# Kernel optimization log

Hardware: AMD Instinct MI355X
Metric: run time of the kernel (lower is better)

The kernel has to match this reference:

```python
import jax, jax.numpy as jnp
import numpy as np
from jax.scipy.linalg import lu_factor, lu_solve

DT = 0.1          # dt
EPS = 0.01        # epsilon
STEPS = 40        # max sweep iterations
TOL = 1e-4        # convergence tolerance


def setup_inputs() -> dict:
    key = jax.random.key(0)
    ks = jax.random.split(key, 9)
    B, D_IN, U, D_OUT = 2048, 1024, 1024, 1000
    def lin(kw, kb, out_f, in_f):
        bound = 1.0 / np.sqrt(in_f)
        W = jax.random.uniform(kw, (out_f, in_f), jnp.float32, -bound, bound)
        b = jax.random.uniform(kb, (out_f,), jnp.float32, -bound, bound)
        return W, b
    x = jax.random.normal(ks[0], (B, D_IN), jnp.float32)
    W_in, b_in = lin(ks[1], ks[2], U, D_IN)
    W1, b1 = lin(ks[3], ks[4], U, U)
    W2, b2 = lin(ks[5], ks[6], U, U)
    W_out, b_out = lin(ks[7], ks[8], D_OUT, U)
    return {"x": x, "W_in": W_in, "b_in": b_in, "W1": W1, "b1": b1,
            "W2": W2, "b2": b2, "W_out": W_out, "b_out": b_out}


def _make_A(W):
    # A = [[I, dt*W], [-dt*W^T, (1+dt/eps)*I]], shape [2u, 2u]
    u = W.shape[0]
    I = jnp.eye(u, dtype=W.dtype)
    return jnp.block([[I, DT * W], [-DT * W.T, (1.0 + DT / EPS) * I]])


def _run_sweep(z_in, rhs1, rhs2, A1, A2):
    # Gauss-Seidel-like sweeping: z1 = A1^{-1}(rhs1+z_in); z2 = A2^{-1}(rhs2+z1)
    # A is identical across the batch, so factor once and solve for all rhs.
    lu1 = lu_factor(A1)
    lu2 = lu_factor(A2)
    r1 = rhs1 + z_in  # constant across sweeps
    def cond(c):
        _, _, err, step = c
        return (step < STEPS) & (err > TOL)
    def body(c):
        z1, z2, _, step = c
        y1 = lu_solve(lu1, r1.T).T
        e1 = jnp.mean(jnp.linalg.norm(z1 - y1, axis=1))
        y2 = lu_solve(lu2, (rhs2 + y1).T).T
        e2 = jnp.mean(jnp.linalg.norm(z2 - y2, axis=1))
        return y1, y2, 0.5 * (e1 + e2), step + 1
    z1, z2, _, _ = jax.lax.while_loop(
        cond, body, (z_in, z_in, jnp.float32(10.0), jnp.int32(0)))
    return z1, z2


@jax.custom_vjp
def _hook(z, A):
    # Forward identity; backward replaces grad g with A^{-T} g (per-row),
    # mirroring the torch register_hook(torch.solve(grad, J^T)).
    return z

def _hook_fwd(z, A):
    return z, A

def _hook_bwd(A, g):
    gz = jnp.linalg.solve(A.T, g.T).T
    return gz, jnp.zeros_like(A)

_hook.defvjp(_hook_fwd, _hook_bwd)


def _implicit(z_in_blk, z_l, W, b, A):
    u = W.shape[0]
    u_in, v_in = z_in_blk[:, :u], z_in_blk[:, u:]
    u_out = u_in + DT * b - DT * (z_l[:, u:] @ W.T)
    v_out = v_in + DT * (z_l[:, :u] @ W) - (DT / EPS) * (z_l[:, u:] - jnp.tanh(u_in))
    z = jnp.concatenate([u_out, v_out], axis=1)
    return _hook(z, jax.lax.stop_gradient(A))


def reference(x, W_in, b_in, W1, b1, W2, b2, W_out, b_out):
    sg = jax.lax.stop_gradient
    u = W1.shape[0]
    B = x.shape[0]
    h = x @ W_in.T + b_in                       # [B, u]
    z_in = jnp.concatenate([h, jnp.tanh(h)], axis=1)  # [B, 2u]
    A1 = _make_A(W1)
    A2 = _make_A(W2)
    # relax rhs = [dt*b, dt/eps * tanh(u_in)] (built from z_in for both blocks)
    tz = (DT / EPS) * jnp.tanh(z_in[:, :u])
    rhs1 = jnp.concatenate([jnp.broadcast_to(DT * b1, (B, u)), tz], axis=1)
    rhs2 = jnp.concatenate([jnp.broadcast_to(DT * b2, (B, u)), tz], axis=1)
    # sweep loop runs under no_grad in the original -> stop_gradient everywhere
    z1, z2 = _run_sweep(sg(z_in), sg(rhs1), sg(rhs2), sg(A1), sg(A2))
    z = _implicit(z_in, z1, W1, b1, A1)
    z = _implicit(z, z2, W2, b2, A2)
    logits = z[:, :u] @ W_out.T + b_out
    return jax.nn.softmax(logits, axis=1)
```

## Files before the change

### kernel.cpp

```cpp
#include <hip/hip_runtime.h>


typedef short bf16x8 __attribute__((ext_vector_type(8)));
typedef float f32x4 __attribute__((ext_vector_type(4)));

#define M1 1048576

__device__ __forceinline__ unsigned short f2b(float f) {
  union { float f; unsigned int u; } v; v.f = f;
  unsigned int u = v.u;
  return (unsigned short)((u + 0x7FFFu + ((u >> 16) & 1u)) >> 16);
}

__device__ __forceinline__ void gload16(const void* g, void* l) {
  __builtin_amdgcn_global_load_lds(
      (const __attribute__((address_space(1))) unsigned int*)g,
      (__attribute__((address_space(3))) unsigned int*)l, 16, 0, 0);
}

template <int MODE, int NKT>
__device__ __forceinline__ void gemm64(
    const unsigned short* __restrict__ A, int lda,
    const unsigned short* __restrict__ B, int ldb,
    int bx, int by,
    const float* bias0, const float* bias1, const float* src0,
    float* dstf0, float* dstf1,
    unsigned short* dstbf, int ldc, unsigned short* dstbf2,
    short (*As)[4096], short (*Bs)[4096]) {
  const int tid = threadIdx.x;
  const int lane = tid & 63;
  const int wid = tid >> 6;
  const int wr = wid >> 1;
  const int wc = wid & 1;
  const int m0 = bx * 64;
  const int n0 = by * 64;
  const int l15 = lane & 15;
  const int kb = lane >> 4;

  const int sr = tid >> 3;
  const int sg = ((tid & 7) - sr) & 7;
  const unsigned short* Asrc = A + (size_t)(m0 + sr) * lda + sg * 8;
  const unsigned short* Bsrc = B + (size_t)(n0 + sr) * ldb + sg * 8;
  const size_t a32 = (size_t)32 * lda;
  const size_t b32 = (size_t)32 * ldb;
  const int o0 = tid * 8;
  const int o1 = 2048 + tid * 8;

  f32x4 acc[2][2];
#pragma unroll
  for (int f = 0; f < 2; ++f)
#pragma unroll
    for (int g = 0; g < 2; ++g) acc[f][g] = (f32x4){0.f, 0.f, 0.f, 0.f};

#define STG(kt, buf)                                  \
  do {                                                \
    gload16(Asrc + (kt) * 64, &As[(buf)][o0]);        \
    gload16(Asrc + a32 + (kt) * 64, &As[(buf)][o1]);  \
    gload16(Bsrc + (kt) * 64, &Bs[(buf)][o0]);        \
    gload16(Bsrc + b32 + (kt) * 64, &Bs[(buf)][o1]);  \
  } while (0)

#define CMP(kt)                                                                \
  do {                                                                         \
    const int cb = (kt) & 3;                                                   \
    bf16x8 av[2][2], bv[2][2];                                                 \
    _Pragma("unroll") for (int f = 0; f < 2; ++f) {                            \
      const int ra = wr * 32 + f * 16 + l15;                                   \
      _Pragma("unroll") for (int ks = 0; ks < 2; ++ks) {                       \
        const int qa = (ks * 4 + kb + l15) & 7;                                \
        av[f][ks] = *reinterpret_cast<const bf16x8*>(&As[cb][ra * 64 + qa * 8]); \
      }                                                                        \
    }                                                                          \
    _Pragma("unroll") for (int g = 0; g < 2; ++g) {                            \
      const int rb = wc * 32 + g * 16 + l15;                                   \
      _Pragma("unroll") for (int ks = 0; ks < 2; ++ks) {                       \
        const int qb2 = (ks * 4 + kb + l15) & 7;                               \
        bv[g][ks] = *reinterpret_cast<const bf16x8*>(&Bs[cb][rb * 64 + qb2 * 8]); \
      }                                                                        \
    }                                                                          \
    _Pragma("unroll") for (int ks = 0; ks < 2; ++ks)                           \
        _Pragma("unroll") for (int f = 0; f < 2; ++f)                          \
            _Pragma("unroll") for (int g = 0; g < 2; ++g)                      \
                acc[f][g] = __builtin_amdgcn_mfma_f32_16x16x32_bf16(           \
                    av[f][ks], bv[g][ks], acc[f][g], 0, 0, 0);                 \
  } while (0)

  STG(0, 0);
  STG(1, 1);

#pragma unroll
  for (int s = 0; s < NKT / 2; ++s) {
    const int k0 = 2 * s;
    asm volatile("s_waitcnt vmcnt(0)" ::: "memory");
    __builtin_amdgcn_sched_barrier(0);
    __builtin_amdgcn_s_barrier();
    __builtin_amdgcn_sched_barrier(0);
    if (k0 + 2 < NKT) STG(k0 + 2, (k0 + 2) & 3);
    if (k0 + 3 < NKT) STG(k0 + 3, (k0 + 3) & 3);
    __builtin_amdgcn_s_setprio(1);
    CMP(k0);
    CMP(k0 + 1);
    __builtin_amdgcn_s_setprio(0);
  }
#undef STG
#undef CMP

#pragma unroll
  for (int f = 0; f < 2; ++f) {
#pragma unroll
    for (int g = 0; g < 2; ++g) {
#pragma unroll
      for (int j = 0; j < 4; ++j) {
        int m = m0 + wr * 32 + f * 16 + kb * 4 + j;
        int n = n0 + wc * 32 + g * 16 + l15;
        size_t fidx = (size_t)m * 1024 + n;
        size_t cidx = (size_t)m * ldc + n;
        float v = acc[f][g][j];
        if (MODE == 0) {
          dstbf[cidx] = f2b(v);
        } else if (MODE == 1) {
          float h = v + bias0[n];
          float thv = tanhf(h);
          float r = h + 0.1f * bias1[n];
          dstf0[fidx] = r;
          dstf1[fidx] = thv;
          dstbf[cidx] = f2b(r);
        } else if (MODE == 2) {
          dstbf[cidx] = f2b(11.0f * src0[fidx] + 0.1f * v);
        } else if (MODE == 4) {
          float r = src0[fidx] + 0.1f * bias0[n] - 0.1f * v;
          dstf0[fidx] = r;
          dstbf[cidx] = f2b(0.1f * r);
        } else if (MODE == 5) {
          dstbf[cidx] = f2b(10.0f * src0[fidx] + v);
        } else if (MODE == 7) {
          dstbf[cidx] = f2b(src0[fidx] - 0.1f * v);
        } else if (MODE == 8) {
          dstf0[fidx] = v + bias0[n];
        } else {
          float q = (m == n ? (1.0f / 11.0f) : 0.0f) - (0.01f / 121.0f) * v;
          unsigned short qq = f2b(q);
          dstbf[cidx] = qq;
          if (dstbf2) dstbf2[(size_t)m * 2048 + n] = qq;
        }
      }
    }
  }
}

__device__ __forceinline__ void map512(int b, int& bx, int& by) {
  bx = ((b & 7) << 2) | ((b >> 3) & 3);
  by = b >> 5;
}
__device__ __forceinline__ void map256(int r, int& bx, int& by) {
  bx = ((r & 7) << 1) | ((r >> 3) & 1);
  by = (r >> 4) & 15;
}
__device__ __forceinline__ void map512k2(int b, int& bx, int& by) {
  const int x = b & 7;
  const int j = b >> 3;
  bx = ((x & 3) << 3) | (j & 7);
  by = ((x >> 2) << 3) | (j >> 3);
}

__global__ __launch_bounds__(256) void k_D2(
    const unsigned short* __restrict__ xb, const unsigned short* __restrict__ winb,
    const unsigned short* __restrict__ wtb,
    const float* __restrict__ b_in, const float* __restrict__ b1,
    float* __restrict__ r1u, float* __restrict__ th,
    unsigned short* __restrict__ zb0, unsigned short* __restrict__ qb,
    unsigned short* __restrict__ bcat) {
  __shared__ short As[4][4096];
  __shared__ short Bs[4][4096];
  const int b = blockIdx.x;
  int bx, by;
  if (b < 512) {
    map512(b, bx, by);
    gemm64<1, 16>(xb, 1024, winb, 1024, bx, by, b_in, b1, nullptr,
                  r1u, th, zb0, 1024, nullptr, As, Bs);
  } else {
    int r = b - 512;
    const int z = r >> 8;
    map256(r & 255, bx, by);
    const unsigned short* wt = wtb + (size_t)z * M1;
    gemm64<9, 16>(wt, 1024, wt, 1024, bx, by, nullptr, nullptr, nullptr,
                  nullptr, nullptr, qb + (size_t)z * M1, 1024,
                  z == 0 ? bcat : nullptr, As, Bs);
  }
}

__global__ __launch_bounds__(256) void k_D3(
    const unsigned short* __restrict__ wb, const unsigned short* __restrict__ qb,
    const unsigned short* __restrict__ zb0, const unsigned short* __restrict__ wtb,
    const float* __restrict__ th,
    unsigned short* __restrict__ a1b, unsigned short* __restrict__ a2b,
    unsigned short* __restrict__ zcat) {
  __shared__ short As[4][4096];
  __shared__ short Bs[4][4096];
  const int b = blockIdx.x;
  int bx, by;
  if (b < 512) {
    const int z = b >> 8;
    map256(b & 255, bx, by);
    gemm64<0, 16>(wb + (size_t)z * M1, 1024, qb + (size_t)z * M1, 1024, bx, by,
                  nullptr, nullptr, nullptr, nullptr, nullptr,
                  z == 0 ? a1b : a2b, 1024, nullptr, As, Bs);
  } else {
    map512(b - 512, bx, by);
    gemm64<2, 16>(zb0, 1024, wtb, 1024, bx, by, nullptr, nullptr, th,
                  nullptr, nullptr, zcat, 2048, nullptr, As, Bs);
  }
}

__global__ __launch_bounds__(256) void k_D4(
    const unsigned short* __restrict__ zcat, const unsigned short* __restrict__ a1b,
    const float* __restrict__ b2, const float* __restrict__ r1u,
    float* __restrict__ r2u, unsigned short* __restrict__ zcat_hi) {
  __shared__ short As[4][4096];
  __shared__ short Bs[4][4096];
  int bx, by;
  map512(blockIdx.x, bx, by);
  gemm64<4, 16>(zcat, 2048, a1b, 1024, bx, by, b2, nullptr, r1u,
                r2u, nullptr, zcat_hi, 2048, nullptr, As, Bs);
}

__global__ __launch_bounds__(256) void k_D5(
    const unsigned short* __restrict__ zcat, const unsigned short* __restrict__ bcat,
    const float* __restrict__ th, unsigned short* __restrict__ zb2) {
  __shared__ short As[4][4096];
  __shared__ short Bs[4][4096];
  int bx, by;
  map512k2(blockIdx.x, bx, by);
  gemm64<5, 32>(zcat, 2048, bcat, 2048, bx, by, nullptr, nullptr, th,
                nullptr, nullptr, zb2, 1024, nullptr, As, Bs);
}

__global__ __launch_bounds__(256) void k_D6(
    const unsigned short* __restrict__ zb2, const unsigned short* __restrict__ a2b,
    const float* __restrict__ r2u, unsigned short* __restrict__ zb3) {
  __shared__ short As[4][4096];
  __shared__ short Bs[4][4096];
  int bx, by;
  map512(blockIdx.x, bx, by);
  gemm64<7, 16>(zb2, 1024, a2b, 1024, bx, by, nullptr, nullptr, r2u,
                nullptr, nullptr, zb3, 1024, nullptr, As, Bs);
}

__global__ __launch_bounds__(256) void k_D7(
    const unsigned short* __restrict__ zb3, const unsigned short* __restrict__ woutb,
    const float* __restrict__ boutp, float* __restrict__ lgts) {
  __shared__ short As[4][4096];
  __shared__ short Bs[4][4096];
  int bx, by;
  map512(blockIdx.x, bx, by);
  gemm64<8, 16>(zb3, 1024, woutb, 1024, bx, by, boutp, nullptr, nullptr,
                lgts, nullptr, nullptr, 1024, nullptr, As, Bs);
}

__global__ __launch_bounds__(256) void k_prep(
    const float* __restrict__ x, const float* __restrict__ Win,
    const float* __restrict__ W1, const float* __restrict__ W2,
    const float* __restrict__ Wout, const float* __restrict__ bout,
    unsigned short* __restrict__ xb, unsigned short* __restrict__ winb,
    unsigned short* __restrict__ wb, unsigned short* __restrict__ wtb,
    unsigned short* __restrict__ woutb, float* __restrict__ boutp,
    unsigned short* __restrict__ bcat) {
  __shared__ float tile[32][33];
  const int b = blockIdx.x;
  const int tid = threadIdx.x;
  if (b < 2048) {
    const int isW2 = (b >> 10) & 1;
    const float* W = isW2 ? W2 : W1;
    unsigned short* Wb = wb + ((size_t)isW2 << 20);
    unsigned short* WTb = wtb + ((size_t)isW2 << 20);
    const int rem = b & 1023;
    const int tbx = rem & 31, tby = rem >> 5;
    const int tx = tid & 31, ty = tid >> 5;
#pragma unroll
    for (int i = ty; i < 32; i += 8) {
      float v = W[(size_t)(tby * 32 + i) * 1024 + tbx * 32 + tx];
      tile[i][tx] = v;
      Wb[(size_t)(tby * 32 + i) * 1024 + tbx * 32 + tx] = f2b(v);
    }
    __syncthreads();
#pragma unroll
    for (int i = ty; i < 32; i += 8) {
      unsigned short t2 = f2b(tile[tx][i]);
      int rr = tbx * 32 + i, cc = tby * 32 + tx;
      WTb[(size_t)rr * 1024 + cc] = t2;
      if (isW2) bcat[(size_t)rr * 2048 + 1024 + cc] = t2;
    }
  } else if (b < 4096) {
    int i = (b - 2048) * 256 + tid;
    float4 v = ((const float4*)x)[i];
    ((ushort4*)xb)[i] = (ushort4){f2b(v.x), f2b(v.y), f2b(v.z), f2b(v.w)};
  } else if (b < 5120) {
    int i = (b - 4096) * 256 + tid;
    float4 v = ((const float4*)Win)[i];
    ((ushort4*)winb)[i] = (ushort4){f2b(v.x), f2b(v.y), f2b(v.z), f2b(v.w)};
  } else if (b < 6144) {
    int i = (b - 5120) * 256 + tid;
    ushort4 o = (ushort4){0, 0, 0, 0};
    if ((i >> 8) < 1000) {
      float4 v = ((const float4*)Wout)[i];
      o = (ushort4){f2b(v.x), f2b(v.y), f2b(v.z), f2b(v.w)};
    }
    ((ushort4*)woutb)[i] = o;
  } else {
    for (int j = tid; j < 1024; j += 256) boutp[j] = (j < 1000) ? bout[j] : 0.0f;
  }
}

__global__ __launch_bounds__(256) void k_softmax(const float* __restrict__ lg,
                                                 float* __restrict__ out) {
  const int r = blockIdx.x;
  const float4* p4 = (const float4*)(lg + (size_t)r * 1024);
  float* q = out + (size_t)r * 1000;
  const int tid = threadIdx.x;
  const int lane = tid & 63;
  const int w = tid >> 6;
  __shared__ float redm[4];
  __shared__ float reds[4];
  float m = -3.0e38f;
  for (int i = tid; i < 250; i += 256) {
    float4 v = p4[i];
    m = fmaxf(fmaxf(fmaxf(m, v.x), fmaxf(v.y, v.z)), v.w);
  }
#pragma unroll
  for (int o = 32; o > 0; o >>= 1) m = fmaxf(m, __shfl_xor(m, o));
  if (lane == 0) redm[w] = m;
  __syncthreads();
  m = fmaxf(fmaxf(redm[0], redm[1]), fmaxf(redm[2], redm[3]));
  float s = 0.0f;
  for (int i = tid; i < 250; i += 256) {
    float4 v = p4[i];
    float e0 = __expf(v.x - m), e1 = __expf(v.y - m);
    float e2 = __expf(v.z - m), e3 = __expf(v.w - m);
    float4 e = {e0, e1, e2, e3};
    *reinterpret_cast<float4*>(q + i * 4) = e;
    s += e0 + e1 + e2 + e3;
  }
#pragma unroll
  for (int o = 32; o > 0; o >>= 1) s += __shfl_xor(s, o);
  if (lane == 0) reds[w] = s;
  __syncthreads();
  float inv = 1.0f / (reds[0] + reds[1] + reds[2] + reds[3]);
  for (int i = tid; i < 250; i += 256) {
    float4 e = *reinterpret_cast<const float4*>(q + i * 4);
    e.x *= inv; e.y *= inv; e.z *= inv; e.w *= inv;
    *reinterpret_cast<float4*>(q + i * 4) = e;
  }
}

extern "C" void kernel_launch(void* const* d_in, const int* in_sizes, int n_in,
                              void* d_out, int out_size, void* d_ws, size_t ws_size,
                              hipStream_t stream) {
  const float* x = (const float*)d_in[0];
  const float* W_in = (const float*)d_in[1];
  const float* b_in = (const float*)d_in[2];
  const float* W1 = (const float*)d_in[3];
  const float* b1 = (const float*)d_in[4];
  const float* W2 = (const float*)d_in[5];
  const float* b2 = (const float*)d_in[6];
  const float* W_out = (const float*)d_in[7];
  const float* b_out = (const float*)d_in[8];
  float* out = (float*)d_out;

  const size_t Bm = 2048, U = 1024;
  char* ws = (char*)d_ws;
  size_t off = 0;
  auto alloc = [&](size_t bytes) -> void* {
    void* p = ws + off;
    off += (bytes + 255) & ~(size_t)255;
    return p;
  };
  unsigned short* xb = (unsigned short*)alloc(Bm * U * 2);
  unsigned short* winb = (unsigned short*)alloc((size_t)M1 * 2);
  unsigned short* wb = (unsigned short*)alloc(2 * (size_t)M1 * 2);
  unsigned short* wtb = (unsigned short*)alloc(2 * (size_t)M1 * 2);
  unsigned short* qb = (unsigned short*)alloc(2 * (size_t)M1 * 2);
  unsigned short* a1b = (unsigned short*)alloc((size_t)M1 * 2);
  unsigned short* a2b = (unsigned short*)alloc((size_t)M1 * 2);
  unsigned short* bcat = (unsigned short*)alloc(2 * (size_t)M1 * 2);
  unsigned short* woutb = (unsigned short*)alloc((size_t)M1 * 2);
  float* boutp = (float*)alloc(U * 4);
  unsigned short* zb0 = (unsigned short*)alloc(Bm * U * 2);
  unsigned short* zcat = (unsigned short*)alloc(Bm * 2 * U * 2);
  unsigned short* zb2 = (unsigned short*)alloc(Bm * U * 2);
  unsigned short* zb3 = (unsigned short*)alloc(Bm * U * 2);
  float* r1u = (float*)alloc(Bm * U * 4);
  float* th = (float*)alloc(Bm * U * 4);
  float* r2u = (float*)alloc(Bm * U * 4);
  float* lgts = (float*)alloc(Bm * U * 4);

  k_prep<<<6145, 256, 0, stream>>>(x, W_in, W1, W2, W_out, b_out,
                                   xb, winb, wb, wtb, woutb, boutp, bcat);
  k_D2<<<1024, 256, 0, stream>>>(xb, winb, wtb, b_in, b1, r1u, th, zb0, qb, bcat);
  k_D3<<<1024, 256, 0, stream>>>(wb, qb, zb0, wtb, th, a1b, a2b, zcat);
  k_D4<<<512, 256, 0, stream>>>(zcat, a1b, b2, r1u, r2u, zcat + 1024);
  k_D5<<<512, 256, 0, stream>>>(zcat, bcat, th, zb2);
  k_D6<<<512, 256, 0, stream>>>(zb2, a2b, r2u, zb3);
  k_D7<<<512, 256, 0, stream>>>(zb3, woutb, boutp, lgts);
  k_softmax<<<2048, 256, 0, stream>>>(lgts, out);
}
```

Before: 105.7 us.

## Split K across wave pairs in 64x64 GEMM tile with LDS reduction

Warps were previously laid out 2x2 over the output tile, each covering 32x32 and all of K. Now each wave pair splits the 64-wide K slice in half, with each wave covering a 64x32 output region over its half of K. The partial sums are then reduced through LDS before a single wave pair runs the epilogue. This cuts the number of LDS fragment reads for each MFMA, since each A fragment is reused across two B fragments and each B across four A fragments. The cost is more accumulator registers, an extra LDS round trip with two barriers, and an epilogue run by only half the waves.

```diff
diff --git a/kernel.cpp b/kernel.cpp
--- a/kernel.cpp
+++ b/kernel.cpp
@@ -30,7 +30,7 @@
   const int tid = threadIdx.x;
   const int lane = tid & 63;
   const int wid = tid >> 6;
-  const int wr = wid >> 1;
+  const int ksw = wid >> 1;
   const int wc = wid & 1;
   const int m0 = bx * 64;
   const int n0 = by * 64;
@@ -46,9 +46,9 @@
   const int o0 = tid * 8;
   const int o1 = 2048 + tid * 8;
 
-  f32x4 acc[2][2];
-#pragma unroll
-  for (int f = 0; f < 2; ++f)
+  f32x4 acc[4][2];
+#pragma unroll
+  for (int f = 0; f < 4; ++f)
 #pragma unroll
     for (int g = 0; g < 2; ++g) acc[f][g] = (f32x4){0.f, 0.f, 0.f, 0.f};
 
@@ -63,26 +63,21 @@
 #define CMP(kt)                                                                \
   do {                                                                         \
     const int cb = (kt) & 3;                                                   \
-    bf16x8 av[2][2], bv[2][2];                                                 \
-    _Pragma("unroll") for (int f = 0; f < 2; ++f) {                            \
-      const int ra = wr * 32 + f * 16 + l15;                                   \
-      _Pragma("unroll") for (int ks = 0; ks < 2; ++ks) {                       \
-        const int qa = (ks * 4 + kb + l15) & 7;                                \
-        av[f][ks] = *reinterpret_cast<const bf16x8*>(&As[cb][ra * 64 + qa * 8]); \
-      }                                                                        \
+    bf16x8 av[4], bv[2];                                                       \
+    _Pragma("unroll") for (int f = 0; f < 4; ++f) {                            \
+      const int ra = f * 16 + l15;                                             \
+      const int qa = (ksw * 4 + kb + l15) & 7;                                 \
+      av[f] = *reinterpret_cast<const bf16x8*>(&As[cb][ra * 64 + qa * 8]);     \
     }                                                                          \
     _Pragma("unroll") for (int g = 0; g < 2; ++g) {                            \
       const int rb = wc * 32 + g * 16 + l15;                                   \
-      _Pragma("unroll") for (int ks = 0; ks < 2; ++ks) {                       \
-        const int qb2 = (ks * 4 + kb + l15) & 7;                               \
-        bv[g][ks] = *reinterpret_cast<const bf16x8*>(&Bs[cb][rb * 64 + qb2 * 8]); \
-      }                                                                        \
+      const int qb2 = (ksw * 4 + kb + l15) & 7;                                \
+      bv[g] = *reinterpret_cast<const bf16x8*>(&Bs[cb][rb * 64 + qb2 * 8]);    \
     }                                                                          \
-    _Pragma("unroll") for (int ks = 0; ks < 2; ++ks)                           \
-        _Pragma("unroll") for (int f = 0; f < 2; ++f)                          \
-            _Pragma("unroll") for (int g = 0; g < 2; ++g)                      \
-                acc[f][g] = __builtin_amdgcn_mfma_f32_16x16x32_bf16(           \
-                    av[f][ks], bv[g][ks], acc[f][g], 0, 0, 0);                 \
+    _Pragma("unroll") for (int f = 0; f < 4; ++f)                              \
+        _Pragma("unroll") for (int g = 0; g < 2; ++g)                          \
+            acc[f][g] = __builtin_amdgcn_mfma_f32_16x16x32_bf16(               \
+                av[f], bv[g], acc[f][g], 0, 0, 0);                             \
   } while (0)
 
   STG(0, 0);
@@ -105,43 +100,61 @@
 #undef STG
 #undef CMP
 
-#pragma unroll
-  for (int f = 0; f < 2; ++f) {
-#pragma unroll
-    for (int g = 0; g < 2; ++g) {
-#pragma unroll
-      for (int j = 0; j < 4; ++j) {
-        int m = m0 + wr * 32 + f * 16 + kb * 4 + j;
-        int n = n0 + wc * 32 + g * 16 + l15;
-        size_t fidx = (size_t)m * 1024 + n;
-        size_t cidx = (size_t)m * ldc + n;
-        float v = acc[f][g][j];
-        if (MODE == 0) {
-          dstbf[cidx] = f2b(v);
-        } else if (MODE == 1) {
-          float h = v + bias0[n];
-          float thv = tanhf(h);
-          float r = h + 0.1f * bias1[n];
-          dstf0[fidx] = r;
-          dstf1[fidx] = thv;
-          dstbf[cidx] = f2b(r);
-        } else if (MODE == 2) {
-          dstbf[cidx] = f2b(11.0f * src0[fidx] + 0.1f * v);
-        } else if (MODE == 4) {
-          float r = src0[fidx] + 0.1f * bias0[n] - 0.1f * v;
-          dstf0[fidx] = r;
-          dstbf[cidx] = f2b(0.1f * r);
-        } else if (MODE == 5) {
-          dstbf[cidx] = f2b(10.0f * src0[fidx] + v);
-        } else if (MODE == 7) {
-          dstbf[cidx] = f2b(src0[fidx] - 0.1f * v);
-        } else if (MODE == 8) {
-          dstf0[fidx] = v + bias0[n];
-        } else {
-          float q = (m == n ? (1.0f / 11.0f) : 0.0f) - (0.01f / 121.0f) * v;
-          unsigned short qq = f2b(q);
-          dstbf[cidx] = qq;
-          if (dstbf2) dstbf2[(size_t)m * 2048 + n] = qq;
+  f32x4* fbuf = reinterpret_cast<f32x4*>(&As[0][0]);
+  __syncthreads();
+  if (ksw == 1) {
+#pragma unroll
+    for (int f = 0; f < 4; ++f)
+#pragma unroll
+      for (int g = 0; g < 2; ++g)
+        fbuf[wc * 512 + (f * 2 + g) * 64 + lane] = acc[f][g];
+  }
+  __syncthreads();
+  if (ksw == 0) {
+#pragma unroll
+    for (int f = 0; f < 4; ++f)
+#pragma unroll
+      for (int g = 0; g < 2; ++g)
+        acc[f][g] += fbuf[wc * 512 + (f * 2 + g) * 64 + lane];
+
+#pragma unroll
+    for (int f = 0; f < 4; ++f) {
+#pragma unroll
+      for (int g = 0; g < 2; ++g) {
+#pragma unroll
+        for (int j = 0; j < 4; ++j) {
+          int m = m0 + f * 16 + kb * 4 + j;
+          int n = n0 + wc * 32 + g * 16 + l15;
+          size_t fidx = (size_t)m * 1024 + n;
+          size_t cidx = (size_t)m * ldc + n;
+          float v = acc[f][g][j];
+          if (MODE == 0) {
+            dstbf[cidx] = f2b(v);
+          } else if (MODE == 1) {
+            float h = v + bias0[n];
+            float thv = tanhf(h);
+            float r = h + 0.1f * bias1[n];
+            dstf0[fidx] = r;
+            dstf1[fidx] = thv;
+            dstbf[cidx] = f2b(r);
+          } else if (MODE == 2) {
+            dstbf[cidx] = f2b(11.0f * src0[fidx] + 0.1f * v);
+          } else if (MODE == 4) {
+            float r = src0[fidx] + 0.1f * bias0[n] - 0.1f * v;
+            dstf0[fidx] = r;
+            dstbf[cidx] = f2b(0.1f * r);
+          } else if (MODE == 5) {
+            dstbf[cidx] = f2b(10.0f * src0[fidx] + v);
+          } else if (MODE == 7) {
+            dstbf[cidx] = f2b(src0[fidx] - 0.1f * v);
+          } else if (MODE == 8) {
+            dstf0[fidx] = v + bias0[n];
+          } else {
+            float q = (m == n ? (1.0f / 11.0f) : 0.0f) - (0.01f / 121.0f) * v;
+            unsigned short qq = f2b(q);
+            dstbf[cidx] = qq;
+            if (dstbf2) dstbf2[(size_t)m * 2048 + n] = qq;
+          }
         }
       }
     }
```

Result: slower. 111.7 us (+5.7%).

## Widen GEMM tiles to 64x128 with 512-thread blocks and 3-stage prefetch

Applied to the files above, without the earlier changes.

Each GEMM block now covers a 64x128 output tile using 8 waves instead of 64x64 with 4 waves. Every A tile load is therefore shared by twice as many columns, and the block count is halved. The K pipeline becomes a triple-buffered ring of paired K-steps with a partial vmcnt wait, so one stage of loads stays in flight while computing. Block-to-tile mappings are rewritten for the new grid. The cost is much more LDS per block (about 144KB), which allows only one block per CU, and fewer blocks than CUs on the 256-block launches, which risks under-filling the GPU.

```diff
diff --git a/kernel.cpp b/kernel.cpp
--- a/kernel.cpp
+++ b/kernel.cpp
@@ -19,32 +19,30 @@
 }
 
 template <int MODE, int NKT>
-__device__ __forceinline__ void gemm64(
+__device__ __forceinline__ void gemm128(
     const unsigned short* __restrict__ A, int lda,
     const unsigned short* __restrict__ B, int ldb,
     int bx, int by,
     const float* bias0, const float* bias1, const float* src0,
     float* dstf0, float* dstf1,
     unsigned short* dstbf, int ldc, unsigned short* dstbf2,
-    short (*As)[4096], short (*Bs)[4096]) {
+    short (*As)[4096], short (*Bs)[8192]) {
   const int tid = threadIdx.x;
   const int lane = tid & 63;
   const int wid = tid >> 6;
-  const int wr = wid >> 1;
-  const int wc = wid & 1;
+  const int wr = wid >> 2;
+  const int wc = wid & 3;
   const int m0 = bx * 64;
-  const int n0 = by * 64;
+  const int n0 = by * 128;
   const int l15 = lane & 15;
   const int kb = lane >> 4;
 
   const int sr = tid >> 3;
   const int sg = ((tid & 7) - sr) & 7;
   const unsigned short* Asrc = A + (size_t)(m0 + sr) * lda + sg * 8;
-  const unsigned short* Bsrc = B + (size_t)(n0 + sr) * ldb + sg * 8;
-  const size_t a32 = (size_t)32 * lda;
-  const size_t b32 = (size_t)32 * ldb;
-  const int o0 = tid * 8;
-  const int o1 = 2048 + tid * 8;
+  const unsigned short* Bsrc0 = B + (size_t)(n0 + sr) * ldb + sg * 8;
+  const unsigned short* Bsrc1 = Bsrc0 + (size_t)64 * ldb;
+  const int od = tid * 8;
 
   f32x4 acc[2][2];
 #pragma unroll
@@ -52,57 +50,60 @@
 #pragma unroll
     for (int g = 0; g < 2; ++g) acc[f][g] = (f32x4){0.f, 0.f, 0.f, 0.f};
 
-#define STG(kt, buf)                                  \
-  do {                                                \
-    gload16(Asrc + (kt) * 64, &As[(buf)][o0]);        \
-    gload16(Asrc + a32 + (kt) * 64, &As[(buf)][o1]);  \
-    gload16(Bsrc + (kt) * 64, &Bs[(buf)][o0]);        \
-    gload16(Bsrc + b32 + (kt) * 64, &Bs[(buf)][o1]);  \
+#define STGP(p)                                                 \
+  do {                                                          \
+    _Pragma("unroll") for (int q = 0; q < 2; ++q) {             \
+      const int kt = 2 * (p) + q;                               \
+      const int sl = ((p) % 3) * 2 + q;                         \
+      gload16(Asrc + kt * 64, &As[sl][od]);                     \
+      gload16(Bsrc0 + kt * 64, &Bs[sl][od]);                    \
+      gload16(Bsrc1 + kt * 64, &Bs[sl][4096 + od]);             \
+    }                                                           \
   } while (0)
 
-#define CMP(kt)                                                                \
+#define CMP(kt, sl)                                                            \
   do {                                                                         \
-    const int cb = (kt) & 3;                                                   \
-    bf16x8 av[2][2], bv[2][2];                                                 \
-    _Pragma("unroll") for (int f = 0; f < 2; ++f) {                            \
-      const int ra = wr * 32 + f * 16 + l15;                                   \
-      _Pragma("unroll") for (int ks = 0; ks < 2; ++ks) {                       \
+    _Pragma("unroll") for (int ks = 0; ks < 2; ++ks) {                         \
+      bf16x8 av[2], bv[2];                                                     \
+      _Pragma("unroll") for (int f = 0; f < 2; ++f) {                          \
+        const int ra = wr * 32 + f * 16 + l15;                                 \
         const int qa = (ks * 4 + kb + l15) & 7;                                \
-        av[f][ks] = *reinterpret_cast<const bf16x8*>(&As[cb][ra * 64 + qa * 8]); \
+        av[f] = *reinterpret_cast<const bf16x8*>(&As[sl][ra * 64 + qa * 8]);   \
       }                                                                        \
+      _Pragma("unroll") for (int g = 0; g < 2; ++g) {                          \
+        const int rb = wc * 32 + g * 16 + l15;                                 \
+        const int qb2 = (ks * 4 + kb + l15) & 7;                               \
+        bv[g] = *reinterpret_cast<const bf16x8*>(&Bs[sl][rb * 64 + qb2 * 8]);  \
+      }                                                                        \
+      _Pragma("unroll") for (int f = 0; f < 2; ++f)                            \
+          _Pragma("unroll") for (int g = 0; g < 2; ++g)                        \
+              acc[f][g] = __builtin_amdgcn_mfma_f32_16x16x32_bf16(             \
+                  av[f], bv[g], acc[f][g], 0, 0, 0);                           \
     }                                                                          \
-    _Pragma("unroll") for (int g = 0; g < 2; ++g) {                            \
-      const int rb = wc * 32 + g * 16 + l15;                                   \
-      _Pragma("unroll") for (int ks = 0; ks < 2; ++ks) {                       \
-        const int qb2 = (ks * 4 + kb + l15) & 7;                               \
-        bv[g][ks] = *reinterpret_cast<const bf16x8*>(&Bs[cb][rb * 64 + qb2 * 8]); \
-      }                                                                        \
-    }                                                                          \
-    _Pragma("unroll") for (int ks = 0; ks < 2; ++ks)                           \
-        _Pragma("unroll") for (int f = 0; f < 2; ++f)                          \
-            _Pragma("unroll") for (int g = 0; g < 2; ++g)                      \
-                acc[f][g] = __builtin_amdgcn_mfma_f32_16x16x32_bf16(           \
-                    av[f][ks], bv[g][ks], acc[f][g], 0, 0, 0);                 \
   } while (0)
 
-  STG(0, 0);
-  STG(1, 1);
-
-#pragma unroll
-  for (int s = 0; s < NKT / 2; ++s) {
-    const int k0 = 2 * s;
-    asm volatile("s_waitcnt vmcnt(0)" ::: "memory");
+  constexpr int NP = NKT / 2;
+  STGP(0);
+  STGP(1);
+
+#pragma unroll
+  for (int s = 0; s < NP; ++s) {
+    if (s + 1 < NP) {
+      asm volatile("s_waitcnt vmcnt(6)" ::: "memory");
+    } else {
+      asm volatile("s_waitcnt vmcnt(0)" ::: "memory");
+    }
     __builtin_amdgcn_sched_barrier(0);
     __builtin_amdgcn_s_barrier();
     __builtin_amdgcn_sched_barrier(0);
-    if (k0 + 2 < NKT) STG(k0 + 2, (k0 + 2) & 3);
-    if (k0 + 3 < NKT) STG(k0 + 3, (k0 + 3) & 3);
+    if (s + 2 < NP) STGP(s + 2);
+    const int sb = (s % 3) * 2;
     __builtin_amdgcn_s_setprio(1);
-    CMP(k0);
-    CMP(k0 + 1);
+    CMP(2 * s, sb);
+    CMP(2 * s + 1, sb + 1);
     __builtin_amdgcn_s_setprio(0);
   }
-#undef STG
+#undef STGP
 #undef CMP
 
 #pragma unroll
@@ -148,113 +149,109 @@
   }
 }
 
-__device__ __forceinline__ void map512(int b, int& bx, int& by) {
-  bx = ((b & 7) << 2) | ((b >> 3) & 3);
-  by = b >> 5;
-}
-__device__ __forceinline__ void map256(int r, int& bx, int& by) {
-  bx = ((r & 7) << 1) | ((r >> 3) & 1);
-  by = (r >> 4) & 15;
-}
-__device__ __forceinline__ void map512k2(int b, int& bx, int& by) {
+__device__ __forceinline__ void mapc(int b, int& bx, int& by) {
   const int x = b & 7;
   const int j = b >> 3;
   bx = ((x & 3) << 3) | (j & 7);
-  by = ((x >> 2) << 3) | (j >> 3);
-}
-
-__global__ __launch_bounds__(256) void k_D2(
+  by = ((x >> 2) << 2) | (j >> 3);
+}
+
+__global__ __launch_bounds__(512) void k_D2(
     const unsigned short* __restrict__ xb, const unsigned short* __restrict__ winb,
     const unsigned short* __restrict__ wtb,
     const float* __restrict__ b_in, const float* __restrict__ b1,
     float* __restrict__ r1u, float* __restrict__ th,
     unsigned short* __restrict__ zb0, unsigned short* __restrict__ qb,
     unsigned short* __restrict__ bcat) {
-  __shared__ short As[4][4096];
-  __shared__ short Bs[4][4096];
+  __shared__ short As[6][4096];
+  __shared__ short Bs[6][8192];
   const int b = blockIdx.x;
   int bx, by;
-  if (b < 512) {
-    map512(b, bx, by);
-    gemm64<1, 16>(xb, 1024, winb, 1024, bx, by, b_in, b1, nullptr,
-                  r1u, th, zb0, 1024, nullptr, As, Bs);
+  if (b < 256) {
+    mapc(b, bx, by);
+    gemm128<1, 16>(xb, 1024, winb, 1024, bx, by, b_in, b1, nullptr,
+                   r1u, th, zb0, 1024, nullptr, As, Bs);
   } else {
-    int r = b - 512;
-    const int z = r >> 8;
-    map256(r & 255, bx, by);
+    int r = b - 256;
+    const int z = r >> 7;
+    r &= 127;
+    const int qbx = r & 15;
+    const int qby = r >> 4;
     const unsigned short* wt = wtb + (size_t)z * M1;
-    gemm64<9, 16>(wt, 1024, wt, 1024, bx, by, nullptr, nullptr, nullptr,
-                  nullptr, nullptr, qb + (size_t)z * M1, 1024,
-                  z == 0 ? bcat : nullptr, As, Bs);
-  }
-}
-
-__global__ __launch_bounds__(256) void k_D3(
+    gemm128<9, 16>(wt, 1024, wt, 1024, qbx, qby, nullptr, nullptr, nullptr,
+                   nullptr, nullptr, qb + (size_t)z * M1, 1024,
+                   z == 0 ? bcat : nullptr, As, Bs);
+  }
+}
+
+__global__ __launch_bounds__(512) void k_D3(
     const unsigned short* __restrict__ wb, const unsigned short* __restrict__ qb,
     const unsigned short* __restrict__ zb0, const unsigned short* __restrict__ wtb,
     const float* __restrict__ th,
     unsigned short* __restrict__ a1b, unsigned short* __restrict__ a2b,
     unsigned short* __restrict__ zcat) {
-  __shared__ short As[4][4096];
-  __shared__ short Bs[4][4096];
+  __shared__ short As[6][4096];
+  __shared__ short Bs[6][8192];
   const int b = blockIdx.x;
-  int bx, by;
-  if (b < 512) {
-    const int z = b >> 8;
-    map256(b & 255, bx, by);
-    gemm64<0, 16>(wb + (size_t)z * M1, 1024, qb + (size_t)z * M1, 1024, bx, by,
-                  nullptr, nullptr, nullptr, nullptr, nullptr,
-                  z == 0 ? a1b : a2b, 1024, nullptr, As, Bs);
+  if (b < 256) {
+    const int z = b >> 7;
+    const int r = b & 127;
+    const int bx = r & 15;
+    const int by = r >> 4;
+    gemm128<0, 16>(wb + (size_t)z * M1, 1024, qb + (size_t)z * M1, 1024, bx, by,
+                   nullptr, nullptr, nullptr, nullptr, nullptr,
+                   z == 0 ? a1b : a2b, 1024, nullptr, As, Bs);
   } else {
-    map512(b - 512, bx, by);
-    gemm64<2, 16>(zb0, 1024, wtb, 1024, bx, by, nullptr, nullptr, th,
-                  nullptr, nullptr, zcat, 2048, nullptr, As, Bs);
-  }
-}
-
-__global__ __launch_bounds__(256) void k_D4(
+    int bx, by;
+    mapc(b - 256, bx, by);
+    gemm128<2, 16>(zb0, 1024, wtb, 1024, bx, by, nullptr, nullptr, th,
+                   nullptr, nullptr, zcat, 2048, nullptr, As, Bs);
+  }
+}
+
+__global__ __launch_bounds__(512) void k_D4(
     const unsigned short* __restrict__ zcat, const unsigned short* __restrict__ a1b,
     const float* __restrict__ b2, const float* __restrict__ r1u,
     float* __restrict__ r2u, unsigned short* __restrict__ zcat_hi) {
-  __shared__ short As[4][4096];
-  __shared__ short Bs[4][4096];
+  __shared__ short As[6][4096];
+  __shared__ short Bs[6][8192];
   int bx, by;
-  map512(blockIdx.x, bx, by);
-  gemm64<4, 16>(zcat, 2048, a1b, 1024, bx, by, b2, nullptr, r1u,
-                r2u, nullptr, zcat_hi, 2048, nullptr, As, Bs);
-}
-
-__global__ __launch_bounds__(256) void k_D5(
+  mapc(blockIdx.x, bx, by);
+  gemm128<4, 16>(zcat, 2048, a1b, 1024, bx, by, b2, nullptr, r1u,
+                 r2u, nullptr, zcat_hi, 2048, nullptr, As, Bs);
+}
+
+__global__ __launch_bounds__(512) void k_D5(
     const unsigned short* __restrict__ zcat, const unsigned short* __restrict__ bcat,
     const float* __restrict__ th, unsigned short* __restrict__ zb2) {
-  __shared__ short As[4][4096];
-  __shared__ short Bs[4][4096];
+  __shared__ short As[6][4096];
+  __shared__ short Bs[6][8192];
   int bx, by;
-  map512k2(blockIdx.x, bx, by);
-  gemm64<5, 32>(zcat, 2048, bcat, 2048, bx, by, nullptr, nullptr, th,
-                nullptr, nullptr, zb2, 1024, nullptr, As, Bs);
-}
-
-__global__ __launch_bounds__(256) void k_D6(
+  mapc(blockIdx.x, bx, by);
+  gemm128<5, 32>(zcat, 2048, bcat, 2048, bx, by, nullptr, nullptr, th,
+                 nullptr, nullptr, zb2, 1024, nullptr, As, Bs);
+}
+
+__global__ __launch_bounds__(512) void k_D6(
     const unsigned short* __restrict__ zb2, const unsigned short* __restrict__ a2b,
     const float* __restrict__ r2u, unsigned short* __restrict__ zb3) {
-  __shared__ short As[4][4096];
-  __shared__ short Bs[4][4096];
+  __shared__ short As[6][4096];
+  __shared__ short Bs[6][8192];
   int bx, by;
-  map512(blockIdx.x, bx, by);
-  gemm64<7, 16>(zb2, 1024, a2b, 1024, bx, by, nullptr, nullptr, r2u,
-                nullptr, nullptr, zb3, 1024, nullptr, As, Bs);
-}
-
-__global__ __launch_bounds__(256) void k_D7(
+  mapc(blockIdx.x, bx, by);
+  gemm128<7, 16>(zb2, 1024, a2b, 1024, bx, by, nullptr, nullptr, r2u,
+                 nullptr, nullptr, zb3, 1024, nullptr, As, Bs);
+}
+
+__global__ __launch_bounds__(512) void k_D7(
     const unsigned short* __restrict__ zb3, const unsigned short* __restrict__ woutb,
     const float* __restrict__ boutp, float* __restrict__ lgts) {
-  __shared__ short As[4][4096];
-  __shared__ short Bs[4][4096];
+  __shared__ short As[6][4096];
+  __shared__ short Bs[6][8192];
   int bx, by;
-  map512(blockIdx.x, bx, by);
-  gemm64<8, 16>(zb3, 1024, woutb, 1024, bx, by, boutp, nullptr, nullptr,
-                lgts, nullptr, nullptr, 1024, nullptr, As, Bs);
+  mapc(blockIdx.x, bx, by);
+  gemm128<8, 16>(zb3, 1024, woutb, 1024, bx, by, boutp, nullptr, nullptr,
+                 lgts, nullptr, nullptr, 1024, nullptr, As, Bs);
 }
 
 __global__ __launch_bounds__(256) void k_prep(
@@ -395,11 +392,11 @@
 
   k_prep<<<6145, 256, 0, stream>>>(x, W_in, W1, W2, W_out, b_out,
                                    xb, winb, wb, wtb, woutb, boutp, bcat);
-  k_D2<<<1024, 256, 0, stream>>>(xb, winb, wtb, b_in, b1, r1u, th, zb0, qb, bcat);
-  k_D3<<<1024, 256, 0, stream>>>(wb, qb, zb0, wtb, th, a1b, a2b, zcat);
-  k_D4<<<512, 256, 0, stream>>>(zcat, a1b, b2, r1u, r2u, zcat + 1024);
-  k_D5<<<512, 256, 0, stream>>>(zcat, bcat, th, zb2);
-  k_D6<<<512, 256, 0, stream>>>(zb2, a2b, r2u, zb3);
-  k_D7<<<512, 256, 0, stream>>>(zb3, woutb, boutp, lgts);
+  k_D2<<<512, 512, 0, stream>>>(xb, winb, wtb, b_in, b1, r1u, th, zb0, qb, bcat);
+  k_D3<<<512, 512, 0, stream>>>(wb, qb, zb0, wtb, th, a1b, a2b, zcat);
+  k_D4<<<256, 512, 0, stream>>>(zcat, a1b, b2, r1u, r2u, zcat + 1024);
+  k_D5<<<256, 512, 0, stream>>>(zcat, bcat, th, zb2);
+  k_D6<<<256, 512, 0, stream>>>(zb2, a2b, r2u, zb3);
+  k_D7<<<256, 512, 0, stream>>>(zb3, woutb, boutp, lgts);
   k_softmax<<<2048, 256, 0, stream>>>(lgts, out);
 }
```

After: 102.5 us (median of 2 runs). 1.03x faster.
